# Kernel optimization log

Hardware: AMD Instinct MI355X
Metric: run time of the kernel (lower is better)

Reference implementation:

```python
import jax, jax.numpy as jnp
import numpy as np

D_MODEL, N_STATE, L_MAX, BATCH = 512, 64, 2048, 8


def _make_dplr_hippo(n):
    # HiPPO-LegS -> NPLR -> DPLR (Annotated-S4 construction)
    p0 = np.sqrt(1.0 + 2.0 * np.arange(n))
    A = p0[:, None] * p0[None, :]
    A = -(np.tril(A) - np.diag(np.arange(n)))
    p = np.sqrt(np.arange(n) + 0.5)
    S = A + p[:, None] * p[None, :]          # normal part (skew-symmetric + const diag)
    lam_re = np.mean(np.diagonal(S)) * np.ones(n)
    lam_im, V = np.linalg.eigh(S * (-1j))
    p_rot = V.conj().T @ p
    return (lam_re.astype(np.float32), lam_im.astype(np.float32),
            p_rot.real.astype(np.float32), p_rot.imag.astype(np.float32))


def setup_inputs() -> dict:
    key = jax.random.key(0)
    k = jax.random.split(key, 8)
    lam_re, lam_im, p_re, p_im = _make_dplr_hippo(N_STATE)
    dt_min, dt_max = 1e-3, 1e-1
    log_step = (jax.random.uniform(k[0], (D_MODEL,))
                * (np.log(dt_max) - np.log(dt_min)) + np.log(dt_min)).astype(jnp.float32)
    s = 0.5 ** 0.5
    B_re = jax.random.normal(k[1], (D_MODEL, N_STATE), dtype=jnp.float32) * s
    B_im = jax.random.normal(k[2], (D_MODEL, N_STATE), dtype=jnp.float32) * s
    Ct_re = jax.random.normal(k[3], (D_MODEL, N_STATE), dtype=jnp.float32) * s
    Ct_im = jax.random.normal(k[4], (D_MODEL, N_STATE), dtype=jnp.float32) * s
    D = jnp.ones((D_MODEL,), jnp.float32)
    lim = 1.0 / np.sqrt(D_MODEL)
    W = jax.random.uniform(k[5], (D_MODEL, D_MODEL), minval=-lim, maxval=lim, dtype=jnp.float32)
    b = jax.random.uniform(k[6], (D_MODEL,), minval=-lim, maxval=lim, dtype=jnp.float32)
    u = jax.random.normal(k[7], (BATCH, L_MAX, D_MODEL), dtype=jnp.float32)
    return dict(u=u,
                lam_re=jnp.asarray(lam_re), lam_im=jnp.asarray(lam_im),
                p_re=jnp.asarray(p_re), p_im=jnp.asarray(p_im),
                B_re=B_re, B_im=B_im, Ct_re=Ct_re, Ct_im=Ct_im,
                log_step=log_step, D=D, W=W, b=b,
                ln_w=jnp.ones((D_MODEL,), jnp.float32),
                ln_b=jnp.zeros((D_MODEL,), jnp.float32))


def _s4_kernel(lam, p, Bc, Ct, step, L):
    # lam, p: (n,) complex; Bc, Ct: (H, n) complex; step: (H,)
    omega = jnp.exp((-2j * jnp.pi) * (jnp.arange(L) / L))          # (L,) roots of unity
    g = (2.0 / step[:, None]) * ((1.0 - omega) / (1.0 + omega))    # (H, L) bilinear transform
    c = 2.0 / (1.0 + omega)                                        # (L,)
    cauchy = 1.0 / (g[:, :, None] - lam)                           # (H, L, n)
    a0, a1 = Ct.conj(), jnp.conj(p)[None, :]
    b0, b1 = Bc, p[None, :]
    k00 = jnp.einsum('hn,hln->hl', a0 * b0, cauchy)
    k01 = jnp.einsum('hn,hln->hl', a0 * b1, cauchy)
    k10 = jnp.einsum('hn,hln->hl', a1 * b0, cauchy)
    k11 = jnp.einsum('hn,hln->hl', a1 * b1, cauchy)
    at_roots = c * (k00 - k01 * (1.0 / (1.0 + k11)) * k10)         # generating fn at roots
    return jnp.fft.ifft(at_roots, n=L, axis=-1).real               # (H, L) real SSM kernel


def reference(u, lam_re, lam_im, p_re, p_im, B_re, B_im, Ct_re, Ct_im,
              log_step, D, W, b, ln_w, ln_b):
    L = u.shape[1]
    lam = lam_re + 1j * lam_im
    p = p_re + 1j * p_im
    Bc = B_re + 1j * B_im
    Ct = Ct_re + 1j * Ct_im
    K = _s4_kernel(lam, p, Bc, Ct, jnp.exp(log_step), L)           # (H, L)
    # causal (non-circular) convolution via zero-padded FFT
    nfft = 2 * L
    Kf = jnp.fft.rfft(K, n=nfft, axis=-1)                          # (H, L+1)
    Uf = jnp.fft.rfft(u, n=nfft, axis=1)                           # (B, L+1, H)
    y = jnp.fft.irfft(Uf * Kf.T[None], n=nfft, axis=1)[:, :L]      # (B, L, H)
    y = y + D * u                                                  # skip connection
    z = jax.nn.gelu(y, approximate=False)                          # GELU (dropout p=0)
    z = jnp.einsum('blh,oh->blo', z, W) + b                        # Linear(d_model, d_model)
    r = z + u                                                      # residual
    mean = r.mean(-1, keepdims=True)
    var = r.var(-1, keepdims=True)
    return (r - mean) / jnp.sqrt(var + 1e-5) * ln_w + ln_b         # LayerNorm
```

## Files before the change

kernel.cpp:

```cpp
#include <hip/hip_runtime.h>
#include <hip/hip_bf16.h>
#include <math.h>

#define PI_F 3.14159265358979f

typedef __attribute__((ext_vector_type(8))) short bf16x8;
typedef __attribute__((ext_vector_type(4))) float f32x4;
typedef __attribute__((ext_vector_type(2))) float f32x2;

#define DM 512
#define LSEQ 2048
#define NB 8
#define NFFT 4096
#define MTOK (NB*LSEQ)

__device__ __forceinline__ float frcp(float x) { return __builtin_amdgcn_rcpf(x); }

__device__ __forceinline__ float gelu_fast(float y) {
  float t = 0.79788456f * (y + 0.044715f * y * y * y);
  float e = __expf(2.0f * t);
  float th = 1.0f - 2.0f * frcp(e + 1.0f);
  return 0.5f * y * (1.0f + th);
}

__device__ __forceinline__ int PD(int i) { return i + (i >> 5); }
#define LDSN 4224

template<bool INV>
__device__ __forceinline__ void dft8(const float xr[8], const float xi[8],
                                     float yr[8], float yi[8]) {
  const float C = 0.70710678118654752f;
  float t0r=xr[0]+xr[4], t0i=xi[0]+xi[4];
  float t1r=xr[0]-xr[4], t1i=xi[0]-xi[4];
  float t2r=xr[2]+xr[6], t2i=xi[2]+xi[6];
  float t3r=xr[2]-xr[6], t3i=xi[2]-xi[6];
  float it3r = INV ? -t3i : t3i;
  float it3i = INV ?  t3r : -t3r;
  float E0r=t0r+t2r, E0i=t0i+t2i;
  float E2r=t0r-t2r, E2i=t0i-t2i;
  float E1r=t1r+it3r, E1i=t1i+it3i;
  float E3r=t1r-it3r, E3i=t1i-it3i;
  float u0r=xr[1]+xr[5], u0i=xi[1]+xi[5];
  float u1r=xr[1]-xr[5], u1i=xi[1]-xi[5];
  float u2r=xr[3]+xr[7], u2i=xi[3]+xi[7];
  float u3r=xr[3]-xr[7], u3i=xi[3]-xi[7];
  float iu3r = INV ? -u3i : u3i;
  float iu3i = INV ?  u3r : -u3r;
  float O0r=u0r+u2r, O0i=u0i+u2i;
  float O2r=u0r-u2r, O2i=u0i-u2i;
  float O1r=u1r+iu3r, O1i=u1i+iu3i;
  float O3r=u1r-iu3r, O3i=u1i-iu3i;
  float w1r = INV ? C*(O1r-O1i) : C*(O1r+O1i);
  float w1i = INV ? C*(O1r+O1i) : C*(O1i-O1r);
  float w2r = INV ? -O2i : O2i;
  float w2i = INV ?  O2r : -O2r;
  float w3r = INV ? -C*(O3r+O3i) : C*(O3i-O3r);
  float w3i = INV ?  C*(O3r-O3i) : -C*(O3r+O3i);
  yr[0]=E0r+O0r; yi[0]=E0i+O0i;
  yr[4]=E0r-O0r; yi[4]=E0i-O0i;
  yr[1]=E1r+w1r; yi[1]=E1i+w1i;
  yr[5]=E1r-w1r; yi[5]=E1i-w1i;
  yr[2]=E2r+w2r; yi[2]=E2i+w2i;
  yr[6]=E2r-w2r; yi[6]=E2i-w2i;
  yr[3]=E3r+w3r; yi[3]=E3i+w3i;
  yr[7]=E3r-w3r; yi[7]=E3i-w3i;
}

template<bool INV>
__device__ __forceinline__ void dft16(const float xr[16], const float xi[16],
                                      float yr[16], float yi[16]) {
  float exr[8], exi[8], oxr[8], oxi[8];
  #pragma unroll
  for (int m = 0; m < 8; ++m) {
    exr[m]=xr[2*m];   exi[m]=xi[2*m];
    oxr[m]=xr[2*m+1]; oxi[m]=xi[2*m+1];
  }
  float er[8], ei[8], orr[8], oii[8];
  dft8<INV>(exr, exi, er, ei);
  dft8<INV>(oxr, oxi, orr, oii);
  const float KC = 0.92387953251128675f;
  const float KS = 0.38268343236508977f;
  const float KH = 0.70710678118654752f;
  float tr, ti;
  yr[0]=er[0]+orr[0]; yi[0]=ei[0]+oii[0];
  yr[8]=er[0]-orr[0]; yi[8]=ei[0]-oii[0];
  { float a=KC, b=INV?KS:-KS;
    tr=orr[1]*a-oii[1]*b; ti=orr[1]*b+oii[1]*a;
    yr[1]=er[1]+tr; yi[1]=ei[1]+ti; yr[9]=er[1]-tr; yi[9]=ei[1]-ti; }
  { float a=KH, b=INV?KH:-KH;
    tr=orr[2]*a-oii[2]*b; ti=orr[2]*b+oii[2]*a;
    yr[2]=er[2]+tr; yi[2]=ei[2]+ti; yr[10]=er[2]-tr; yi[10]=ei[2]-ti; }
  { float a=KS, b=INV?KC:-KC;
    tr=orr[3]*a-oii[3]*b; ti=orr[3]*b+oii[3]*a;
    yr[3]=er[3]+tr; yi[3]=ei[3]+ti; yr[11]=er[3]-tr; yi[11]=ei[3]-ti; }
  { if (INV) { tr=-oii[4]; ti= orr[4]; } else { tr= oii[4]; ti=-orr[4]; }
    yr[4]=er[4]+tr; yi[4]=ei[4]+ti; yr[12]=er[4]-tr; yi[12]=ei[4]-ti; }
  { float a=-KS, b=INV?KC:-KC;
    tr=orr[5]*a-oii[5]*b; ti=orr[5]*b+oii[5]*a;
    yr[5]=er[5]+tr; yi[5]=ei[5]+ti; yr[13]=er[5]-tr; yi[13]=ei[5]-ti; }
  { float a=-KH, b=INV?KH:-KH;
    tr=orr[6]*a-oii[6]*b; ti=orr[6]*b+oii[6]*a;
    yr[6]=er[6]+tr; yi[6]=ei[6]+ti; yr[14]=er[6]-tr; yi[14]=ei[6]-ti; }
  { float a=-KC, b=INV?KS:-KS;
    tr=orr[7]*a-oii[7]*b; ti=orr[7]*b+oii[7]*a;
    yr[7]=er[7]+tr; yi[7]=ei[7]+ti; yr[15]=er[7]-tr; yi[15]=ei[7]-ti; }
}

template<bool INV, int NSLOG, int NBF>
__device__ __forceinline__ void r16s(float* sr, float* si, int tid,
                                     float c1, float s1f) {
  float yr[16], yi[16];
  bool act = (NBF >= 256) || (tid < NBF);
  __syncthreads();
  if (act) {
    float xr[16], xi[16];
    #pragma unroll
    for (int m = 0; m < 16; ++m) {
      int ix = PD(tid + m * NBF);
      xr[m] = sr[ix]; xi[m] = si[ix];
    }
    if (NSLOG > 0) {
      float s1 = INV ? -s1f : s1f;
      float wr = c1, wi = s1;
      #pragma unroll
      for (int m = 1; m < 16; ++m) {
        float tr = xr[m]*wr - xi[m]*wi;
        float ti = xr[m]*wi + xi[m]*wr;
        xr[m] = tr; xi[m] = ti;
        float nr = wr*c1 - wi*s1;
        float ni = wr*s1 + wi*c1;
        wr = nr; wi = ni;
      }
    }
    dft16<INV>(xr, xi, yr, yi);
  }
  __syncthreads();
  if (act) {
    int r = tid & ((1 << NSLOG) - 1);
    int q = tid >> NSLOG;
    int base = (q << (NSLOG + 4)) + r;
    #pragma unroll
    for (int p = 0; p < 16; ++p) {
      int ix = PD(base + (p << NSLOG));
      sr[ix] = yr[p]; si[ix] = yi[p];
    }
  }
}

__device__ __forceinline__ void r16s_zfirst(float* sr, float* si, int tid) {
  const float KC = 0.92387953251128675f;
  const float KS = 0.38268343236508977f;
  const float KH = 0.70710678118654752f;
  float xr[8], xi[8];
  __syncthreads();
  #pragma unroll
  for (int m = 0; m < 8; ++m) {
    int ix = PD(tid + m * 256);
    xr[m] = sr[ix]; xi[m] = si[ix];
  }
  float er[8], ei[8];
  dft8<false>(xr, xi, er, ei);
  float tr[8], ti[8];
  tr[0] = xr[0];                      ti[0] = xi[0];
  tr[1] =  xr[1]*KC + xi[1]*KS;       ti[1] =  xi[1]*KC - xr[1]*KS;
  tr[2] = (xr[2] + xi[2])*KH;         ti[2] = (xi[2] - xr[2])*KH;
  tr[3] =  xr[3]*KS + xi[3]*KC;       ti[3] =  xi[3]*KS - xr[3]*KC;
  tr[4] =  xi[4];                     ti[4] = -xr[4];
  tr[5] = -xr[5]*KS + xi[5]*KC;       ti[5] = -xi[5]*KS - xr[5]*KC;
  tr[6] = (xi[6] - xr[6])*KH;         ti[6] = -(xr[6] + xi[6])*KH;
  tr[7] = -xr[7]*KC + xi[7]*KS;       ti[7] = -xi[7]*KC - xr[7]*KS;
  float odr[8], odi[8];
  dft8<false>(tr, ti, odr, odi);
  __syncthreads();
  int base = tid << 4;
  #pragma unroll
  for (int j = 0; j < 8; ++j) {
    int ie = PD(base + 2*j), io = PD(base + 2*j + 1);
    sr[ie] = er[j];  si[ie] = ei[j];
    sr[io] = odr[j]; si[io] = odi[j];
  }
}

template<bool INV, int NSLOG, int NBF>
__device__ __forceinline__ void r8s(float* sr, float* si, int tid,
                                    float c1, float s1f) {
  float yr[8], yi[8];
  bool act = (NBF >= 256) || (tid < NBF);
  __syncthreads();
  if (act) {
    float xr[8], xi[8];
    #pragma unroll
    for (int m = 0; m < 8; ++m) {
      int ix = PD(tid + m * NBF);
      xr[m] = sr[ix]; xi[m] = si[ix];
    }
    if (NSLOG > 0) {
      float s1 = INV ? -s1f : s1f;
      float wr = c1, wi = s1;
      #pragma unroll
      for (int m = 1; m < 8; ++m) {
        float tr = xr[m]*wr - xi[m]*wi;
        float ti = xr[m]*wi + xi[m]*wr;
        xr[m] = tr; xi[m] = ti;
        float nr = wr*c1 - wi*s1;
        float ni = wr*s1 + wi*c1;
        wr = nr; wi = ni;
      }
    }
    dft8<INV>(xr, xi, yr, yi);
  }
  __syncthreads();
  if (act) {
    int r = tid & ((1 << NSLOG) - 1);
    int q = tid >> NSLOG;
    int base = (q << (NSLOG + 3)) + r;
    #pragma unroll
    for (int p = 0; p < 8; ++p) {
      int ix = PD(base + (p << NSLOG));
      sr[ix] = yr[p]; si[ix] = yi[p];
    }
  }
}

template<bool INV>
__device__ __forceinline__ void fft4096(float* sr, float* si, int tid,
                                        float cA, float sA, float cB, float sB) {
  r16s<INV, 0, 256>(sr, si, tid, 1.f, 0.f);
  r16s<INV, 4, 256>(sr, si, tid, cA, sA);
  r16s<INV, 8, 256>(sr, si, tid, cB, sB);
  __syncthreads();
}

__device__ __forceinline__ void fft4096z(float* sr, float* si, int tid,
                                         float cA, float sA, float cB, float sB) {
  r16s_zfirst(sr, si, tid);
  r16s<false, 4, 256>(sr, si, tid, cA, sA);
  r16s<false, 8, 256>(sr, si, tid, cB, sB);
  __syncthreads();
}

template<bool INV>
__device__ __forceinline__ void fft2048(float* sr, float* si, int tid,
                                        float cA, float sA, float cB, float sB) {
  r8s <INV, 0, 256>(sr, si, tid, 1.f, 0.f);
  r16s<INV, 3, 128>(sr, si, tid, cA, sA);
  r16s<INV, 7, 128>(sr, si, tid, cB, sB);
  __syncthreads();
}

__global__ __launch_bounds__(256) void k_prep(
    const float* __restrict__ lam_re, const float* __restrict__ lam_im,
    const float* __restrict__ p_re,   const float* __restrict__ p_im,
    const float* __restrict__ B_re,   const float* __restrict__ B_im,
    const float* __restrict__ Ct_re,  const float* __restrict__ Ct_im,
    float* __restrict__ wtab, float4* __restrict__ otab) {
  int bidx = blockIdx.x;
  if (bidx < 128) {
    int idx = bidx * 256 + threadIdx.x;
    int n = idx & 63;
    float br = B_re[idx],  bi = B_im[idx];
    float cr = Ct_re[idx], ci = Ct_im[idx];
    float pr = p_re[n],    pi = p_im[n];
    float* w = wtab + (size_t)idx * 12;
    w[0] = cr*br + ci*bi;   w[1] = cr*bi - ci*br;
    w[2] = cr*pr + ci*pi;   w[3] = cr*pi - ci*pr;
    w[4] = pr*br + pi*bi;   w[5] = pr*bi - pi*br;
    w[6] = pr*pr + pi*pi;   w[7] = lam_re[n];
    w[8] = lam_im[n];       w[9] = 0.f; w[10] = 0.f; w[11] = 0.f;
  } else {
    int l = (bidx - 128) * 256 + threadIdx.x;
    float omi, omr;
    sincosf(-2.0f * PI_F * (float)l / (float)LSEQ, &omi, &omr);
    float a = 1.0f + omr;
    float iv = frcp(a*a + omi*omi);
    float4 o;
    o.x = 2.0f * a * iv;
    o.y = -2.0f * omi * iv;
    o.z = (1.0f - omr*omr - omi*omi) * iv;
    o.w = (-2.0f * omi) * iv;
    otab[l] = o;
  }
}

__global__ __launch_bounds__(256) void k_mega(
    const float* __restrict__ wtab, const float4* __restrict__ otab,
    const float* __restrict__ log_step, float2* __restrict__ atr,
    const float* __restrict__ u, float* __restrict__ ut,
    const float* __restrict__ W, __hip_bfloat16* __restrict__ Wb) {
  __shared__ float tsh[32][33];
  int bidx = blockIdx.x;
  int tid = threadIdx.x;
  if (bidx < 2048) {
    int h = bidx >> 2;
    int l0 = ((bidx & 3) << 8) + tid;
    int l1 = l0 + 1024;
    float tos = 2.0f * expf(-log_step[h]);
    float4 o0 = otab[l0];
    float4 o1 = otab[l1];
    float cr0 = o0.x, ci0 = o0.y, cr1 = o1.x, ci1 = o1.y;
    f32x2 gr, gi;
    gr.x = tos * o0.z;  gr.y = tos * o1.z;
    gi.x = tos * o0.w;  gi.y = tos * o1.w;
    f32x2 K00r={0.f,0.f},K00i={0.f,0.f},K01r={0.f,0.f},K01i={0.f,0.f},
          K10r={0.f,0.f},K10i={0.f,0.f},K11r={0.f,0.f},K11i={0.f,0.f};
    const float4* wq = (const float4*)(wtab + (size_t)h * 64 * 12);
    #pragma unroll 8
    for (int n = 0; n < 64; ++n) {
      float4 wa = wq[n*3+0];
      float4 wb = wq[n*3+1];
      float  lim = wq[n*3+2].x;
      f32x2 dr = gr - wb.w;
      f32x2 di = gi - lim;
      f32x2 den = dr*dr + di*di;
      float ip = frcp(den.x * den.y);
      f32x2 inv; inv.x = den.y * ip; inv.y = den.x * ip;
      f32x2 car = dr*inv, cai = -di*inv;
      K00r += wa.x*car - wa.y*cai;  K00i += wa.x*cai + wa.y*car;
      K01r += wa.z*car - wa.w*cai;  K01i += wa.z*cai + wa.w*car;
      K10r += wb.x*car - wb.y*cai;  K10i += wb.x*cai + wb.y*car;
      K11r += wb.z*car;             K11i += wb.z*cai;
    }
    {
      float tr = K01r.x*K10r.x - K01i.x*K10i.x, ti = K01r.x*K10i.x + K01i.x*K10r.x;
      float d1r = 1.0f + K11r.x, d1i = K11i.x;
      float invd1 = frcp(d1r*d1r + d1i*d1i);
      float t2r = (tr*d1r + ti*d1i) * invd1;
      float t2i = (ti*d1r - tr*d1i) * invd1;
      float numr = K00r.x - t2r, numi = K00i.x - t2i;
      atr[(size_t)h * LSEQ + l0] = make_float2(cr0*numr - ci0*numi, cr0*numi + ci0*numr);
    }
    {
      float tr = K01r.y*K10r.y - K01i.y*K10i.y, ti = K01r.y*K10i.y + K01i.y*K10r.y;
      float d1r = 1.0f + K11r.y, d1i = K11i.y;
      float invd1 = frcp(d1r*d1r + d1i*d1i);
      float t2r = (tr*d1r + ti*d1i) * invd1;
      float t2i = (ti*d1r - tr*d1i) * invd1;
      float numr = K00r.y - t2r, numi = K00i.y - t2i;
      atr[(size_t)h * LSEQ + l1] = make_float2(cr1*numr - ci1*numi, cr1*numi + ci1*numr);
    }
  } else if (bidx < 2048 + 8192) {
    int t = bidx - 2048;
    int lx = t & 63, hy = (t >> 6) & 15, b = t >> 10;
    int l0 = lx * 32, h0 = hy * 32;
    int x = tid & 31, y0 = tid >> 5;
    #pragma unroll
    for (int i = 0; i < 4; ++i) {
      int y = y0 + i*8;
      tsh[y][x] = u[((size_t)b*LSEQ + l0 + y) * DM + h0 + x];
    }
    __syncthreads();
    #pragma unroll
    for (int i = 0; i < 4; ++i) {
      int y = y0 + i*8;
      ut[((size_t)b*DM + h0 + y) * LSEQ + l0 + x] = tsh[x][y];
    }
  } else {
    int i = (bidx - 10240) * 256 + tid;
    Wb[i] = __float2bfloat16(W[i]);
  }
}

__global__ __launch_bounds__(256, 4) void k_fftK(const float2* __restrict__ atr,
                                                 float2* __restrict__ Kf) {
  __shared__ float sr[LDSN], si[LDSN];
  int h = blockIdx.x, tid = threadIdx.x;
  float c2a, s2a, c2b, s2b, c4a, s4a, c4b, s4b;
  { int r = tid & 7;   __sincosf(-2.f*PI_F*(float)r/128.f,  &s2a, &c2a); }
  { int r = tid & 127; __sincosf(-2.f*PI_F*(float)r/2048.f, &s2b, &c2b); }
  { int r = tid & 15;  __sincosf(-2.f*PI_F*(float)r/256.f,  &s4a, &c4a); }
  { int r = tid;       __sincosf(-2.f*PI_F*(float)r/4096.f, &s4b, &c4b); }
  const float2* ap = atr + (size_t)h * LSEQ;
  #pragma unroll
  for (int i = 0; i < 8; ++i) {
    int l = tid + i*256;
    float2 v = ap[l];
    sr[PD(l)] = v.x; si[PD(l)] = v.y;
  }
  fft2048<true>(sr, si, tid, c2a, s2a, c2b, s2b);
  #pragma unroll
  for (int i = 0; i < 8; ++i) {
    int m = tid + i*256;
    float v = sr[PD(m)] * (1.0f / (float)LSEQ);
    sr[PD(m)] = v;
    si[PD(m)] = 0.0f;
  }
  fft4096z(sr, si, tid, c4a, s4a, c4b, s4b);
  float2* ko = Kf + (size_t)h * NFFT;
  #pragma unroll
  for (int i = 0; i < 16; ++i) {
    int f = tid + i*256;
    ko[f] = make_float2(sr[PD(f)], si[PD(f)]);
  }
}

__global__ __launch_bounds__(256, 4) void k_conv(const float* __restrict__ ut,
                                                 const float2* __restrict__ Kf,
                                                 const float* __restrict__ Dvec,
                                                 __hip_bfloat16* __restrict__ zbt) {
  __shared__ float sr[LDSN], si[LDSN];
  int wg = blockIdx.x;
  int bp = wg >> 9, h = wg & 511;
  int b0 = bp*2, b1 = bp*2 + 1;
  int tid = threadIdx.x;
  float c4a, s4a, c4b, s4b;
  { int r = tid & 15; __sincosf(-2.f*PI_F*(float)r/256.f,  &s4a, &c4a); }
  { int r = tid;      __sincosf(-2.f*PI_F*(float)r/4096.f, &s4b, &c4b); }
  const float* u0p = ut + ((size_t)(b0*DM + h)) * LSEQ;
  const float* u1p = ut + ((size_t)(b1*DM + h)) * LSEQ;
  #pragma unroll
  for (int i = 0; i < 8; ++i) {
    int l = tid + i*256;
    sr[PD(l)] = u0p[l];  si[PD(l)] = u1p[l];
  }
  fft4096z(sr, si, tid, c4a, s4a, c4b, s4b);
  float yrg[16], yig[16];
  const float2* kp = Kf + (size_t)h * NFFT;
  #pragma unroll
  for (int i = 0; i < 16; ++i) {
    int f = tid + i*256;
    int fn = (NFFT - f) & (NFFT - 1);
    float ar = sr[PD(f)],  ai = si[PD(f)];
    float br = sr[PD(fn)], bi = -si[PD(fn)];
    float u0r = 0.5f*(ar + br), u0i = 0.5f*(ai + bi);
    float u1r = 0.5f*(ai - bi), u1i = -0.5f*(ar - br);
    float2 K0 = kp[f];
    float y0r = u0r*K0.x - u0i*K0.y, y0i = u0r*K0.y + u0i*K0.x;
    float y1r = u1r*K0.x - u1i*K0.y, y1i = u1r*K0.y + u1i*K0.x;
    yrg[i] = y0r - y1i;
    yig[i] = y0i + y1r;
  }
  __syncthreads();
  #pragma unroll
  for (int i = 0; i < 16; ++i) {
    int f = tid + i*256;
    sr[PD(f)] = yrg[i]; si[PD(f)] = yig[i];
  }
  fft4096<true>(sr, si, tid, c4a, s4a, c4b, s4b);
  float d = Dvec[h];
  __hip_bfloat16* zb0 = zbt + ((size_t)(b0*DM + h)) * LSEQ;
  __hip_bfloat16* zb1 = zbt + ((size_t)(b1*DM + h)) * LSEQ;
  const float inv_n = 1.0f / (float)NFFT;
  #pragma unroll
  for (int i = 0; i < 8; ++i) {
    int l = tid + i*256;
    float y0 = sr[PD(l)]*inv_n + d*u0p[l];
    float y1 = si[PD(l)]*inv_n + d*u1p[l];
    zb0[l] = __float2bfloat16(gelu_fast(y0));
    zb1[l] = __float2bfloat16(gelu_fast(y1));
  }
}

__global__ __launch_bounds__(512) void k_gemm_ln(
    const ushort* __restrict__ zbt,
    const short* __restrict__ Wb,
    const float* __restrict__ bias,
    const float* __restrict__ u,
    const float* __restrict__ lnw, const float* __restrict__ lnb,
    float* __restrict__ out) {
  __shared__ ushort sA[64][40];
  __shared__ short sB[512][40];
  __shared__ float red[2][4][64];
  __shared__ float smu[64], srs[64];
  __shared__ float sln[2][DM];
  int tid = threadIdx.x, wave = tid >> 6, lane = tid & 63;
  int wm = wave >> 2, wn = wave & 3;
  int m0 = blockIdx.x * 64;
  int b = m0 >> 11;
  int l0 = m0 & (LSEQ - 1);
  const ushort* zb = zbt + (size_t)b * DM * LSEQ;
  int row = lane & 15, kq8 = (lane >> 4) << 3;
  int kk = tid >> 4, seg = tid & 15;
  int cB = (tid & 3) << 3, rB = tid >> 2;
  sln[0][tid] = lnw[tid];
  sln[1][tid] = lnb[tid];
  f32x4 acc[2][8];
  #pragma unroll
  for (int i = 0; i < 2; ++i)
    #pragma unroll
    for (int j = 0; j < 8; ++j) acc[i][j] = (f32x4){0.f,0.f,0.f,0.f};
  for (int k0 = 0; k0 < DM; k0 += 32) {
    __syncthreads();
    {
      uint2 v = *(const uint2*)(zb + (size_t)(k0 + kk)*LSEQ + l0 + seg*4);
      const ushort* p = (const ushort*)&v;
      sA[seg*4 + 0][kk] = p[0];
      sA[seg*4 + 1][kk] = p[1];
      sA[seg*4 + 2][kk] = p[2];
      sA[seg*4 + 3][kk] = p[3];
    }
    #pragma unroll
    for (int jj = 0; jj < 4; ++jj) {
      int o = rB + jj*128;
      *(uint4*)&sB[o][cB] = *(const uint4*)(Wb + (size_t)o*DM + k0 + cB);
    }
    __syncthreads();
    bf16x8 a0 = *(const bf16x8*)&sA[wm*32 + row][kq8];
    bf16x8 a1 = *(const bf16x8*)&sA[wm*32 + 16 + row][kq8];
    #pragma unroll
    for (int nt = 0; nt < 8; ++nt) {
      bf16x8 bf = *(const bf16x8*)&sB[wn*128 + nt*16 + row][kq8];
      acc[0][nt] = __builtin_amdgcn_mfma_f32_16x16x32_bf16(a0, bf, acc[0][nt], 0, 0, 0);
      acc[1][nt] = __builtin_amdgcn_mfma_f32_16x16x32_bf16(a1, bf, acc[1][nt], 0, 0, 0);
    }
  }
  int ccol = lane & 15, crow = (lane >> 4) << 2;
  #pragma unroll
  for (int rt = 0; rt < 2; ++rt) {
    #pragma unroll
    for (int rr = 0; rr < 4; ++rr) {
      int lr = wm*32 + rt*16 + crow + rr;
      int gr = m0 + lr;
      float ls = 0.f, ls2 = 0.f;
      #pragma unroll
      for (int nt = 0; nt < 8; ++nt) {
        int col = wn*128 + nt*16 + ccol;
        float v = acc[rt][nt][rr] + bias[col] + u[(size_t)gr*DM + col];
        acc[rt][nt][rr] = v;
        ls += v; ls2 += v*v;
      }
      ls  += __shfl_xor(ls, 1);  ls2 += __shfl_xor(ls2, 1);
      ls  += __shfl_xor(ls, 2);  ls2 += __shfl_xor(ls2, 2);
      ls  += __shfl_xor(ls, 4);  ls2 += __shfl_xor(ls2, 4);
      ls  += __shfl_xor(ls, 8);  ls2 += __shfl_xor(ls2, 8);
      if (ccol == 0) { red[0][wn][lr] = ls; red[1][wn][lr] = ls2; }
    }
  }
  __syncthreads();
  if (tid < 64) {
    float s = red[0][0][tid] + red[0][1][tid] + red[0][2][tid] + red[0][3][tid];
    float q = red[1][0][tid] + red[1][1][tid] + red[1][2][tid] + red[1][3][tid];
    float mean = s * (1.0f/(float)DM);
    float var  = q * (1.0f/(float)DM) - mean*mean;
    smu[tid] = mean;
    srs[tid] = rsqrtf(var + 1e-5f);
  }
  __syncthreads();
  #pragma unroll
  for (int rt = 0; rt < 2; ++rt) {
    #pragma unroll
    for (int rr = 0; rr < 4; ++rr) {
      int lr = wm*32 + rt*16 + crow + rr;
      int gr = m0 + lr;
      float mu = smu[lr], rs = srs[lr];
      #pragma unroll
      for (int nt = 0; nt < 8; ++nt) {
        int col = wn*128 + nt*16 + ccol;
        out[(size_t)gr*DM + col] = (acc[rt][nt][rr] - mu) * rs * sln[0][col] + sln[1][col];
      }
    }
  }
}

extern "C" void kernel_launch(void* const* d_in, const int* in_sizes, int n_in,
                              void* d_out, int out_size, void* d_ws, size_t ws_size,
                              hipStream_t stream) {
  const float* u        = (const float*)d_in[0];
  const float* lam_re   = (const float*)d_in[1];
  const float* lam_im   = (const float*)d_in[2];
  const float* p_re     = (const float*)d_in[3];
  const float* p_im     = (const float*)d_in[4];
  const float* B_re     = (const float*)d_in[5];
  const float* B_im     = (const float*)d_in[6];
  const float* Ct_re    = (const float*)d_in[7];
  const float* Ct_im    = (const float*)d_in[8];
  const float* log_step = (const float*)d_in[9];
  const float* Dv       = (const float*)d_in[10];
  const float* W        = (const float*)d_in[11];
  const float* bias     = (const float*)d_in[12];
  const float* ln_w     = (const float*)d_in[13];
  const float* ln_b     = (const float*)d_in[14];
  float* out = (float*)d_out;
  char* ws = (char*)d_ws;

  float2* Kf = (float2*)ws;
  float*  ut = (float*)(ws + (16u << 20));
  __hip_bfloat16* zbt = (__hip_bfloat16*)(ws + (48u << 20));
  float2* atr  = (float2*)(ws + (48u << 20));
  float*  wtab = (float*)(ws + (56u << 20));
  float4* otab = (float4*)(ws + (58u << 20));
  __hip_bfloat16* Wb = (__hip_bfloat16*)(ws + (64u << 20));
  if (ws_size < (65u << 20)) return;

  k_prep<<<dim3(136), dim3(256), 0, stream>>>(lam_re, lam_im, p_re, p_im,
                                              B_re, B_im, Ct_re, Ct_im, wtab, otab);
  k_mega<<<dim3(2048 + 8192 + 1024), dim3(256), 0, stream>>>(
      wtab, otab, log_step, atr, u, ut, W, Wb);
  k_fftK<<<dim3(DM), dim3(256), 0, stream>>>(atr, Kf);
  k_conv<<<dim3((NB/2) * DM), dim3(256), 0, stream>>>(ut, Kf, Dv, zbt);
  k_gemm_ln<<<dim3(MTOK/64), dim3(512), 0, stream>>>((const ushort*)zbt, (const short*)Wb,
                                                     bias, u, ln_w, ln_b, out);
}
```

Baseline: 124.8 us.

## Merge transpose and W-cast work into kernel-generation blocks to overlap loads

The mega kernel previously dispatched separate blocks for SSM kernel generation, the u transpose and the W bf16 cast. Now each of 2048 blocks first issues global loads for four transpose tiles and one W element into registers, then does the compute-heavy kernel-generation loop, and finally writes the transposed tiles and the bf16 weights. The aim is to hide memory latency behind the compute loop and cut block count and launch scheduling overhead. The cost is higher register pressure (16 extra floats held across the loop), which may reduce occupancy, plus extra barriers per block.

```diff
diff --git a/kernel.cpp b/kernel.cpp
--- a/kernel.cpp
+++ b/kernel.cpp
@@ -290,7 +290,25 @@
   __shared__ float tsh[32][33];
   int bidx = blockIdx.x;
   int tid = threadIdx.x;
-  if (bidx < 2048) {
+  int x = tid & 31, y0 = tid >> 5;
+
+  float ur[4][4];
+  #pragma unroll
+  for (int t = 0; t < 4; ++t) {
+    int id = bidx*4 + t;
+    int lx = id & 63, hy = (id >> 6) & 15, b = id >> 10;
+    int l0 = lx*32, h0 = hy*32;
+    #pragma unroll
+    for (int i = 0; i < 4; ++i) {
+      int y = y0 + i*8;
+      ur[t][i] = u[((size_t)b*LSEQ + l0 + y)*DM + h0 + x];
+    }
+  }
+  bool doW = bidx < 1024;
+  int wi = bidx*256 + tid;
+  float wv = doW ? W[wi] : 0.0f;
+
+  {
     int h = bidx >> 2;
     int l0 = ((bidx & 3) << 8) + tid;
     int l1 = l0 + 1024;
@@ -338,25 +356,24 @@
       float numr = K00r.y - t2r, numi = K00i.y - t2i;
       atr[(size_t)h * LSEQ + l1] = make_float2(cr1*numr - ci1*numi, cr1*numi + ci1*numr);
     }
-  } else if (bidx < 2048 + 8192) {
-    int t = bidx - 2048;
-    int lx = t & 63, hy = (t >> 6) & 15, b = t >> 10;
-    int l0 = lx * 32, h0 = hy * 32;
-    int x = tid & 31, y0 = tid >> 5;
+  }
+
+  if (doW) Wb[wi] = __float2bfloat16(wv);
+  #pragma unroll
+  for (int t = 0; t < 4; ++t) {
+    int id = bidx*4 + t;
+    int lx = id & 63, hy = (id >> 6) & 15, b = id >> 10;
+    int l0 = lx*32, h0 = hy*32;
+    __syncthreads();
+    #pragma unroll
+    for (int i = 0; i < 4; ++i)
+      tsh[y0 + i*8][x] = ur[t][i];
+    __syncthreads();
     #pragma unroll
     for (int i = 0; i < 4; ++i) {
       int y = y0 + i*8;
-      tsh[y][x] = u[((size_t)b*LSEQ + l0 + y) * DM + h0 + x];
-    }
-    __syncthreads();
-    #pragma unroll
-    for (int i = 0; i < 4; ++i) {
-      int y = y0 + i*8;
-      ut[((size_t)b*DM + h0 + y) * LSEQ + l0 + x] = tsh[x][y];
-    }
-  } else {
-    int i = (bidx - 10240) * 256 + tid;
-    Wb[i] = __float2bfloat16(W[i]);
+      ut[((size_t)b*DM + h0 + y)*LSEQ + l0 + x] = tsh[x][y];
+    }
   }
 }
 
@@ -583,7 +600,7 @@
 
   k_prep<<<dim3(136), dim3(256), 0, stream>>>(lam_re, lam_im, p_re, p_im,
                                               B_re, B_im, Ct_re, Ct_im, wtab, otab);
-  k_mega<<<dim3(2048 + 8192 + 1024), dim3(256), 0, stream>>>(
+  k_mega<<<dim3(2048), dim3(256), 0, stream>>>(
       wtab, otab, log_step, atr, u, ut, W, Wb);
   k_fftK<<<dim3(DM), dim3(256), 0, stream>>>(atr, Kf);
   k_conv<<<dim3((NB/2) * DM), dim3(256), 0, stream>>>(ut, Kf, Dv, zbt);
```

Result: slower. 127.8 us (+2.4%).
